# Optimization experiments

Hardware: AMD Instinct MI355X
Metric: run time of the kernel (lower is better)

Reference implementation:

```python
import jax, jax.numpy as jnp
import numpy as np

BS, C, H, W = 256, 512, 9, 9
D = 9           # spe_kerner (spectral attention kernel size)
SPA_HEAD = 64
HW = H * W      # 81; with spe_head=1, padsize=9 => share_head = 81 = HW
EPS = 1e-5


def _bn(x, p, axis=1):
    # inference-mode BatchNorm; p is (4, C) = [gamma, beta, running_mean, running_var]
    g, b, m, v = p
    sh = [1] * x.ndim; sh[axis] = -1
    return (x - m.reshape(sh)) * (g.reshape(sh) * jax.lax.rsqrt(v.reshape(sh) + EPS)) + b.reshape(sh)


def _conv2d(x, w, groups=1):
    return jax.lax.conv_general_dilated(
        x, w, (1, 1), 'SAME',
        dimension_numbers=('NCHW', 'OIHW', 'NCHW'),
        feature_group_count=groups)


def setup_inputs() -> dict:
    key = jax.random.key(0)
    ks = list(jax.random.split(key, 16))

    def rn(k, shape, s=0.05):
        return (jax.random.normal(k, shape) * s).astype(jnp.float32)

    def bnp(k, c):
        k1, k2, k3, k4 = jax.random.split(k, 4)
        g = jax.random.uniform(k1, (c,), minval=0.5, maxval=1.5)
        v = jax.random.uniform(k4, (c,), minval=0.5, maxval=1.5)
        return jnp.stack([g, rn(k2, (c,)), rn(k3, (c,)), v]).astype(jnp.float32)

    return {
        'x': jax.random.normal(ks[0], (BS, C, H, W), jnp.float32),
        'alpha': jnp.full((1,), 0.5, jnp.float32),
        # SaMCA params
        'sa_key_w': rn(ks[1], (C, 1, 3, 3)),                    # depthwise 3x3 key conv
        'sa_key_bn': bnp(ks[2], C),
        'sa_att_w1': rn(ks[3], (C, 2 * C // SPA_HEAD, 1, 1)),   # Conv2d(2C, C, 1, groups=64)
        'sa_att_bn': bnp(ks[4], C),
        'sa_att_w2': rn(ks[5], (SPA_HEAD, C // SPA_HEAD, 1, 1)),  # Conv2d(C, 64, 1, groups=64)
        'sa_att_b2': rn(ks[6], (SPA_HEAD,)),
        # SeMCA params
        'se_key_w': rn(ks[7], (HW, 1, D)),                      # depthwise Conv1d over spectral axis
        'se_key_b': rn(ks[8], (HW,)),
        'se_att_w1': rn(ks[9], (HW, 2 * HW)),                   # 1x1 Conv2d(162, 81), bias=False
        'se_att_bn': bnp(ks[10], HW),
        'se_att_w2': rn(ks[11], (D, HW)),                       # 1x1 Conv2d(81, 9)
        'se_att_b2': rn(ks[12], (D,)),
        'se_val_w': rn(ks[13], (C, 1, 3, 3)),                   # depthwise 3x3 value conv
        'se_val_b': rn(ks[14], (C,)),
    }


def reference(x, alpha, sa_key_w, sa_key_bn, sa_att_w1, sa_att_bn, sa_att_w2,
              sa_att_b2, se_key_w, se_key_b, se_att_w1, se_att_bn, se_att_w2,
              se_att_b2, se_val_w, se_val_b):
    bs, c, h, w = x.shape
    hw = h * w
    # ================= SeMCA (spectral attention) =================
    # convd_key: depthwise Conv1d over the spectral (channel) axis per pixel
    k = x.reshape(bs, c, hw).transpose(0, 2, 1)                 # (bs, hw, c)
    k1 = jax.lax.conv_general_dilated(
        k, se_key_w, (1,), [(D // 2, D // 2)],
        dimension_numbers=('NCH', 'OIH', 'NCH'),
        feature_group_count=hw) + se_key_b[None, :, None]
    k1 = k1.transpose(0, 2, 1).reshape(bs, c, h, w)
    # With padsize==img_size, Unfold(kernel=9) is a single full window -> flatten.
    q_flat = x.reshape(bs, 1, c * hw)
    k_flat = k1.reshape(bs, 1, c * hw)
    # torch layout-faithful: stack on dim 2 then reshape (bs, 2*hw, c)
    kq = jnp.stack([q_flat, k_flat], axis=2).reshape(bs, 2 * hw, c)
    a = jax.nn.relu(_bn(jnp.einsum('oi,bic->boc', se_att_w1, kq), se_att_bn))
    a = jnp.einsum('oi,bic->boc', se_att_w2, a) + se_att_b2[None, :, None]  # (bs, D, c)
    # repeat over all 81 positions + trivial block reshape (sidelen=1) -> same
    # D-vector at every pixel; softmax over the spectral kernel axis.
    a = jax.nn.softmax(a, axis=1)
    v = _conv2d(x, se_val_w, groups=c) + se_val_b[None, :, None, None]
    pad_v = jnp.pad(v, ((0, 0), (D // 2, D // 2), (0, 0), (0, 0)))
    # spectral sliding windows: v_win[b, i, k] = v_padded[b, i + k - D//2]
    v_win = jnp.stack([pad_v[:, k0:k0 + c] for k0 in range(D)], axis=2)  # (bs,c,D,h,w)
    out1 = jnp.einsum('bcdhw,bdc->bchw', v_win, a) + k1
    # ================= SaMCA (spatial attention) =================
    k1s = jax.nn.relu(_bn(_conv2d(x, sa_key_w, groups=c), sa_key_bn))
    # NOTE: value_embed in the original is computed then overwritten by x (dead code).
    kq2 = jnp.stack([k1s, x], axis=2).reshape(bs, 2 * c, h, w)  # interleaved channels
    a2 = jax.nn.relu(_bn(_conv2d(kq2, sa_att_w1, groups=SPA_HEAD), sa_att_bn))
    a2 = _conv2d(a2, sa_att_w2, groups=SPA_HEAD) + sa_att_b2[None, :, None, None]
    a2 = jax.nn.softmax(a2.reshape(bs, SPA_HEAD, hw), axis=-1)  # global spatial softmax
    k2 = jnp.broadcast_to(a2[:, :, None, :], (bs, SPA_HEAD, c // SPA_HEAD, hw)).reshape(bs, c, hw)
    out2 = k1s + (k2 * x.reshape(bs, c, hw)).reshape(bs, c, h, w)
    return alpha * out1 + (1.0 - alpha) * out2
```

## Files before the change

### kernel.cpp

```cpp
#include <hip/hip_runtime.h>
#include <hip/hip_fp16.h>

#define BSZ 256
#define CCH 512
#define HW_ 81
#define DD 9
#define CH 41472

#define WS_W1T   0
#define WS_TSE   13122
#define WS_S2    13203
#define WS_T2    13715
#define WS_W1S   14227
#define WS_T1    22419
#define WS_A2    22932
#define WS_ATT   1350036
#define WS_W1F   2529684
#define WS_TOTALP 22931
#define PREP_N   41363

typedef _Float16 half8 __attribute__((ext_vector_type(8)));
typedef float f32x4 __attribute__((ext_vector_type(4)));

__device__ __forceinline__ float h2f(unsigned short u) {
    return __half2float(__ushort_as_half(u));
}
__device__ __forceinline__ unsigned short f2h(float f) {
    return __half_as_ushort(__float2half(f));
}

__global__ void prep_kernel(const float* __restrict__ se_att_w1,
                            const float* __restrict__ se_att_bn,
                            const float* __restrict__ sa_key_bn,
                            const float* __restrict__ sa_att_w1,
                            const float* __restrict__ sa_att_bn,
                            float* __restrict__ ws) {
    int idx = blockIdx.x * blockDim.x + threadIdx.x;
    if (idx < 13122) {
        int r = idx / 81, o = idx % 81;
        float g = se_att_bn[o], v = se_att_bn[243 + o];
        float s = g * rsqrtf(v + 1e-5f);
        ws[WS_W1T + idx] = se_att_w1[o * 162 + r] * s;
    } else if (idx < 13203) {
        int o = idx - 13122;
        float g = se_att_bn[o], b = se_att_bn[81 + o], m = se_att_bn[162 + o], v = se_att_bn[243 + o];
        float s = g * rsqrtf(v + 1e-5f);
        ws[WS_TSE + o] = b - m * s;
    } else if (idx < 13715) {
        int c = idx - 13203;
        float g = sa_key_bn[c], v = sa_key_bn[1536 + c];
        ws[WS_S2 + c] = g * rsqrtf(v + 1e-5f);
    } else if (idx < 14227) {
        int c = idx - 13715;
        float g = sa_key_bn[c], b = sa_key_bn[512 + c], m = sa_key_bn[1024 + c], v = sa_key_bn[1536 + c];
        float s = g * rsqrtf(v + 1e-5f);
        ws[WS_T2 + c] = b - m * s;
    } else if (idx < 22419) {
        int e = idx - 14227;
        int o = e >> 4;
        float g = sa_att_bn[o], v = sa_att_bn[1536 + o];
        float s = g * rsqrtf(v + 1e-5f);
        ws[WS_W1S + e] = sa_att_w1[e] * s;
    } else if (idx < WS_TOTALP) {
        int o = idx - 22419;
        float g = sa_att_bn[o], b = sa_att_bn[512 + o], m = sa_att_bn[1024 + o], v = sa_att_bn[1536 + o];
        float s = g * rsqrtf(v + 1e-5f);
        ws[WS_T1 + o] = b - m * s;
    } else if (idx < PREP_N) {
        int e2 = (idx - WS_TOTALP) * 2;
        unsigned int packed = 0;
        #pragma unroll
        for (int q = 0; q < 2; ++q) {
            int e = e2 + q;
            int row = e / 192, k = e - row * 192;
            unsigned short val = 0;
            if (row < 81 && k < 162) {
                float g = se_att_bn[row], v = se_att_bn[243 + row];
                float s = g * rsqrtf(v + 1e-5f);
                val = f2h(se_att_w1[row * 162 + k] * s);
            }
            packed |= ((unsigned int)val) << (16 * q);
        }
        ((unsigned int*)(ws + WS_W1F))[idx - WS_TOTALP] = packed;
    }
}

__global__ __launch_bounds__(512, 4) void sa_kernel(
    const float* __restrict__ x,
    const float* __restrict__ sa_key_w,
    const float* __restrict__ sa_att_w2,
    const float* __restrict__ sa_att_b2,
    float* __restrict__ ws)
{
    __shared__ __align__(16) unsigned short xbh[128 * HW_];
    __shared__ float kvf[128 * HW_];
    __shared__ unsigned short wkbL[128 * DD];
    __shared__ float s2L[128];
    __shared__ float t2L[128];
    __shared__ float w1sL[128 * 16];
    __shared__ float saw2L[128];
    __shared__ float b2L[16];
    __shared__ float t1L[128];

    const int bid = blockIdx.x;
    const int b = bid >> 2;
    const int qr = bid & 3;
    const int c0 = qr * 128;
    const int t = threadIdx.x;

    {
        const float4* x4 = (const float4*)(x + (size_t)b * CH + (size_t)c0 * 81);
        for (int v = t; v < 128 * 81 / 4; v += 512) {
            float4 q = x4[v];
            ushort4 s4;
            s4.x = f2h(q.x); s4.y = f2h(q.y); s4.z = f2h(q.z); s4.w = f2h(q.w);
            *(ushort4*)(&xbh[4 * v]) = s4;
        }
        for (int v = t; v < 128 * DD; v += 512) wkbL[v] = f2h(sa_key_w[c0 * 9 + v]);
        if (t < 128) {
            s2L[t] = ws[WS_S2 + c0 + t];
            t2L[t] = ws[WS_T2 + c0 + t];
            saw2L[t] = sa_att_w2[c0 + t];
            t1L[t] = ws[WS_T1 + c0 + t];
        }
        for (int v = t; v < 128 * 16; v += 512) w1sL[v] = ws[WS_W1S + c0 * 16 + v];
        if (t < 16) b2L[t] = sa_att_b2[qr * 16 + t];
    }
    __syncthreads();

    #pragma unroll 2
    for (int idx = t; idx < 128 * 81; idx += 512) {
        int c = idx / 81, p = idx - 81 * c;
        int y = p / 9, xx = p - 9 * y;
        float conv = 0.f;
        #pragma unroll
        for (int ky = 0; ky < 3; ++ky) {
            int yy = y + ky - 1;
            if (yy < 0 || yy > 8) continue;
            #pragma unroll
            for (int kx = 0; kx < 3; ++kx) {
                int xc = xx + kx - 1;
                if (xc < 0 || xc > 8) continue;
                conv = fmaf(h2f(xbh[c * 81 + yy * 9 + xc]),
                            h2f(wkbL[c * 9 + ky * 3 + kx]), conv);
            }
        }
        kvf[idx] = fmaxf(conv * s2L[c] + t2L[c], 0.f);
    }
    __syncthreads();

    {
        const int g = t >> 5, sub = t & 31;
        const int cb = g * 8;
        float z[8][3];
        #pragma unroll
        for (int o = 0; o < 8; ++o)
            #pragma unroll
            for (int k = 0; k < 3; ++k)
                z[o][k] = t1L[cb + o];

        #pragma unroll 1
        for (int j = 0; j < 8; ++j) {
            float wk[8], wx[8];
            #pragma unroll
            for (int o = 0; o < 8; ++o) {
                wk[o] = w1sL[(cb + o) * 16 + 2 * j];
                wx[o] = w1sL[(cb + o) * 16 + 2 * j + 1];
            }
            const int rowb = (cb + j) * 81;
            #pragma unroll
            for (int k = 0; k < 3; ++k) {
                int p = sub + 32 * k;
                if (p > 80) p = 80;
                float kv = kvf[rowb + p];
                float xv = h2f(xbh[rowb + p]);
                #pragma unroll
                for (int o = 0; o < 8; ++o) {
                    z[o][k] = fmaf(wk[o], kv, z[o][k]);
                    z[o][k] = fmaf(wx[o], xv, z[o][k]);
                }
            }
        }

        float a2v[3];
        const float b2g = b2L[g];
        #pragma unroll
        for (int k = 0; k < 3; ++k) {
            float s = b2g;
            #pragma unroll
            for (int o = 0; o < 8; ++o)
                s = fmaf(saw2L[cb + o], fmaxf(z[o][k], 0.f), s);
            int p = sub + 32 * k;
            a2v[k] = (p < 81) ? s : -1e30f;
        }

        float m = a2v[0];
        #pragma unroll
        for (int k = 1; k < 3; ++k) m = fmaxf(m, a2v[k]);
        #pragma unroll
        for (int off = 1; off < 32; off <<= 1) m = fmaxf(m, __shfl_xor(m, off, 64));
        float ls = 0.f;
        float ev[3];
        #pragma unroll
        for (int k = 0; k < 3; ++k) { ev[k] = __expf(a2v[k] - m); ls += ev[k]; }
        #pragma unroll
        for (int off = 1; off < 32; off <<= 1) ls += __shfl_xor(ls, off, 64);
        float inv = 1.f / ls;

        float* a2out = ws + WS_A2 + (size_t)b * 5184 + (size_t)(qr * 16 + g) * 81;
        #pragma unroll
        for (int k = 0; k < 3; ++k) {
            int p = sub + 32 * k;
            if (p < 81) a2out[p] = ev[k] * inv;
        }
    }
}

__global__ __launch_bounds__(512) void se_kernel(
    const float* __restrict__ x,
    const float* __restrict__ se_key_w,
    const float* __restrict__ se_key_b,
    const float* __restrict__ se_att_w2,
    const float* __restrict__ se_att_b2,
    float* __restrict__ ws)
{
    __shared__ __align__(16) unsigned short xbh[CH];
    __shared__ __align__(16) unsigned short kqs[128 * 200];
    __shared__ float wseL[DD * HW_];
    __shared__ float bseL[HW_];
    __shared__ float w2L[DD * 96];
    __shared__ float tseL[96];

    const int b = blockIdx.x;
    const int t = threadIdx.x;
    const float* xb = x + (size_t)b * CH;

    for (int v = t; v < DD * HW_; v += 512) {
        int tau = v / 81, p = v - 81 * tau;
        wseL[tau * 81 + p] = se_key_w[p * 9 + tau];
    }
    if (t < HW_) bseL[t] = se_key_b[t];
    for (int v = t; v < DD * 96; v += 512) {
        int d = v / 96, row = v - 96 * d;
        w2L[v] = (row < 81) ? se_att_w2[d * 81 + row] : 0.f;
    }
    if (t < 96) tseL[t] = (t < 81) ? ws[WS_TSE + t] : 0.f;
    for (int v = t; v < 128 * 38; v += 512) {
        int k = v >> 7, jl = v & 127;
        kqs[jl * 200 + 162 + k] = 0;
    }
    {
        const float4* x4 = (const float4*)xb;
        #pragma unroll 4
        for (int v = t; v < CH / 4; v += 512) {
            float4 q = x4[v];
            ushort4 s4;
            s4.x = f2h(q.x); s4.y = f2h(q.y); s4.z = f2h(q.z); s4.w = f2h(q.w);
            *(ushort4*)(&xbh[4 * v]) = s4;
        }
    }
    __syncthreads();

    const int wv = t >> 6;
    const int lane = t & 63;
    const int quad = lane >> 4;
    const int l15 = lane & 15;
    const unsigned short* w1f = (const unsigned short*)(ws + WS_W1F);
    float* attout = ws + WS_ATT + (size_t)b * 4608;

    #pragma unroll 1
    for (int q = 0; q < 4; ++q) {
        const int c0 = q * 128;
        if (q) __syncthreads();

        {
            int k = t >> 7;
            const int jl = t & 127;
            #pragma unroll 2
            for (; k < 81; k += 4)
                kqs[jl * 200 + k] = xbh[k * 512 + c0 + jl];
        }
        {
            int kk = t >> 7;
            const int jl = t & 127;
            int e = kk * 512 + c0 + jl;
            int p = e % 81;
            #pragma unroll 2
            for (; kk < 81; kk += 4) {
                float s = bseL[p];
                if (e >= 324 && e < CH - 324) {
                    #pragma unroll
                    for (int tau = 0; tau < 9; ++tau)
                        s = fmaf(h2f(xbh[e - 324 + 81 * tau]), wseL[tau * 81 + p], s);
                } else {
                    #pragma unroll
                    for (int tau = 0; tau < 9; ++tau) {
                        int flat = e + (tau - 4) * 81;
                        if (flat >= 0 && flat < CH)
                            s = fmaf(h2f(xbh[flat]), wseL[tau * 81 + p], s);
                    }
                }
                kqs[jl * 200 + 81 + kk] = f2h(s);
                e += 2048;
                p += 23; if (p >= 81) p -= 81;
            }
        }
        __syncthreads();

        f32x4 acc[6];
        #pragma unroll
        for (int m = 0; m < 6; ++m) acc[m] = (f32x4){0.f, 0.f, 0.f, 0.f};

        #pragma unroll 1
        for (int pass = 0; pass < 6; ++pass) {
            half8 bfr = *(const half8*)&kqs[(wv * 16 + l15) * 200 + pass * 32 + quad * 8];
            #pragma unroll
            for (int m = 0; m < 6; ++m) {
                half8 afr = *(const half8*)&w1f[(m * 16 + l15) * 192 + pass * 32 + quad * 8];
                acc[m] = __builtin_amdgcn_mfma_f32_16x16x32_f16(afr, bfr, acc[m], 0, 0, 0);
            }
        }

        float pd[9];
        #pragma unroll
        for (int d = 0; d < 9; ++d) pd[d] = 0.f;
        #pragma unroll
        for (int m = 0; m < 6; ++m) {
            #pragma unroll
            for (int reg = 0; reg < 4; ++reg) {
                int row = m * 16 + quad * 4 + reg;
                float z = fmaxf(acc[m][reg] + tseL[row], 0.f);
                #pragma unroll
                for (int d = 0; d < 9; ++d)
                    pd[d] = fmaf(w2L[d * 96 + row], z, pd[d]);
            }
        }
        #pragma unroll
        for (int d = 0; d < 9; ++d) {
            pd[d] += __shfl_xor(pd[d], 16, 64);
            pd[d] += __shfl_xor(pd[d], 32, 64);
        }
        if (quad == 0) {
            int j = c0 + wv * 16 + l15;
            float ad[9];
            #pragma unroll
            for (int d = 0; d < 9; ++d) ad[d] = pd[d] + se_att_b2[d];
            float mm = ad[0];
            #pragma unroll
            for (int d = 1; d < 9; ++d) mm = fmaxf(mm, ad[d]);
            float ls = 0.f;
            #pragma unroll
            for (int d = 0; d < 9; ++d) { ad[d] = __expf(ad[d] - mm); ls += ad[d]; }
            float inv = 1.f / ls;
            #pragma unroll
            for (int d = 0; d < 9; ++d) attout[d * 512 + j] = ad[d] * inv;
        }
    }
}

#define CS 108
#define RS 12

__device__ __forceinline__ void ldrow_h(const unsigned short* base, float* r) {
    ushort4 a = *(const ushort4*)(base);
    ushort4 bq = *(const ushort4*)(base + 4);
    unsigned short c = base[8];
    r[0] = h2f(a.x); r[1] = h2f(a.y); r[2] = h2f(a.z); r[3] = h2f(a.w);
    r[4] = h2f(bq.x); r[5] = h2f(bq.y); r[6] = h2f(bq.z); r[7] = h2f(bq.w);
    r[8] = h2f(c);
}
__device__ __forceinline__ void ldrow_f(const float* base, float* r) {
    float4 a = *(const float4*)(base);
    float4 bq = *(const float4*)(base + 4);
    r[0] = a.x; r[1] = a.y; r[2] = a.z; r[3] = a.w;
    r[4] = bq.x; r[5] = bq.y; r[6] = bq.z; r[7] = bq.w;
    r[8] = base[8];
}
__device__ __forceinline__ void zrow(float* r) {
    #pragma unroll
    for (int xx = 0; xx < 9; ++xx) r[xx] = 0.f;
}

__global__ __launch_bounds__(256) void combine_kernel(
    const float* __restrict__ x,
    const float* __restrict__ alpha,
    const float* __restrict__ sa_key_w,
    const float* __restrict__ se_key_w,
    const float* __restrict__ se_key_b,
    const float* __restrict__ se_val_w,
    const float* __restrict__ se_val_b,
    const float* __restrict__ ws,
    float* __restrict__ out)
{
    __shared__ __align__(16) unsigned short xsh[72 * CS];
    __shared__ __align__(16) unsigned short vsh[72 * CS];
    __shared__ __align__(16) float wsePad[9 * CS];
    __shared__ __align__(16) float bsePad[CS];
    __shared__ __align__(16) float a2Pad[8 * CS];
    __shared__ float wvL[72 * 9];
    __shared__ float bvL[72];
    __shared__ float wkL[64 * 9];
    __shared__ float s2L[64];
    __shared__ float t2L[64];
    __shared__ float attL[9 * 64];

    const int bid = blockIdx.x;
    const int b = bid >> 3;
    const int tile = bid & 7;
    const int c0 = tile * 64;
    const int t = threadIdx.x;
    const int f0 = (c0 - 4) * 81;

    {
        const float* xg = x + (size_t)b * CH;
        for (int v4 = t; v4 < 1458; v4 += 256) {
            int lf = v4 * 4;
            int gf = f0 + lf;
            float4 q = (gf >= 0 && gf < CH) ? *(const float4*)(xg + gf)
                                            : (float4){0.f, 0.f, 0.f, 0.f};
            #pragma unroll
            for (int j = 0; j < 4; ++j) {
                int lfj = lf + j;
                int i = lfj / 81, p = lfj - 81 * i;
                int yy = p / 9, xx = p - 9 * yy;
                xsh[i * CS + yy * RS + xx] = f2h(((const float*)&q)[j]);
            }
        }
    }
    for (int idx = t; idx < 648; idx += 256) {
        int cc = c0 - 4 + idx / 9;
        wvL[idx] = (cc >= 0 && cc < 512) ? se_val_w[cc * 9 + idx % 9] : 0.f;
    }
    if (t < 72) {
        int cc = c0 - 4 + t;
        bvL[t] = (cc >= 0 && cc < 512) ? se_val_b[cc] : 0.f;
    }
    for (int idx = t; idx < 576; idx += 256) wkL[idx] = sa_key_w[c0 * 9 + idx];
    if (t < 64) { s2L[t] = ws[WS_S2 + c0 + t]; t2L[t] = ws[WS_T2 + c0 + t]; }
    for (int idx = t; idx < 972; idx += 256) {
        int tau = idx / CS, r = idx - CS * tau;
        int yy = r / RS, xx = r - RS * yy;
        if (xx < 9) wsePad[idx] = se_key_w[(yy * 9 + xx) * 9 + tau];
    }
    if (t < CS) {
        int yy = t / RS, xx = t - RS * yy;
        if (xx < 9) bsePad[t] = se_key_b[yy * 9 + xx];
    }
    for (int idx = t; idx < 864; idx += 256) {
        int g = idx / CS, r = idx - CS * g;
        int yy = r / RS, xx = r - RS * yy;
        if (xx < 9)
            a2Pad[idx] = ws[WS_A2 + (size_t)b * 5184 + (size_t)(tile * 8 + g) * 81 + yy * 9 + xx];
    }
    for (int idx = t; idx < 576; idx += 256)
        attL[idx] = ws[WS_ATT + (size_t)b * 4608 + (idx >> 6) * 512 + c0 + (idx & 63)];
    __syncthreads();

    #pragma unroll 1
    for (int u = t; u < 648; u += 256) {
        int i = u / 9, yy = u - 9 * i;
        const int cb = i * CS;
        float q0[9], q1[9], q2[9];
        if (yy > 0) ldrow_h(&xsh[cb + (yy - 1) * RS], q0);
        else zrow(q0);
        ldrow_h(&xsh[cb + yy * RS], q1);
        if (yy < 8) ldrow_h(&xsh[cb + (yy + 1) * RS], q2);
        else zrow(q2);
        float wv[9];
        #pragma unroll
        for (int j = 0; j < 9; ++j) wv[j] = wvL[i * 9 + j];
        const float bv = bvL[i];
        float o[9];
        #pragma unroll
        for (int xx = 0; xx < 9; ++xx) {
            float s = bv;
            #pragma unroll
            for (int kx = 0; kx < 3; ++kx) {
                int xc = xx + kx - 1;
                if (xc >= 0 && xc <= 8) {
                    s = fmaf(q0[xc], wv[kx], s);
                    s = fmaf(q1[xc], wv[3 + kx], s);
                    s = fmaf(q2[xc], wv[6 + kx], s);
                }
            }
            o[xx] = s;
        }
        const int vb = cb + yy * RS;
        ushort4 wA, wB;
        wA.x = f2h(o[0]); wA.y = f2h(o[1]); wA.z = f2h(o[2]); wA.w = f2h(o[3]);
        wB.x = f2h(o[4]); wB.y = f2h(o[5]); wB.z = f2h(o[6]); wB.w = f2h(o[7]);
        *(ushort4*)(&vsh[vb]) = wA;
        *(ushort4*)(&vsh[vb + 4]) = wB;
        vsh[vb + 8] = f2h(o[8]);
    }
    __syncthreads();

    const float av = alpha[0];
    #pragma unroll 1
    for (int u = t; u < 576; u += 256) {
        int cl = u / 9, yy = u - 9 * cl;
        const int rb = yy * RS;
        float acc[9];
        ldrow_f(&bsePad[rb], acc);
        float r1[9];
        #pragma unroll
        for (int tau = 0; tau < 9; ++tau) {
            float xr[9], wr[9];
            ldrow_h(&xsh[(cl + tau) * CS + rb], xr);
            ldrow_f(&wsePad[tau * CS + rb], wr);
            #pragma unroll
            for (int xx = 0; xx < 9; ++xx) acc[xx] = fmaf(xr[xx], wr[xx], acc[xx]);
            if (tau == 4) {
                #pragma unroll
                for (int xx = 0; xx < 9; ++xx) r1[xx] = xr[xx];
            }
        }
        #pragma unroll
        for (int d = 0; d < 9; ++d) {
            float vr[9];
            ldrow_h(&vsh[(cl + d) * CS + rb], vr);
            const float ad = attL[d * 64 + cl];
            #pragma unroll
            for (int xx = 0; xx < 9; ++xx) acc[xx] = fmaf(vr[xx], ad, acc[xx]);
        }
        float r0[9], r2[9];
        if (yy > 0) ldrow_h(&xsh[(cl + 4) * CS + rb - RS], r0);
        else zrow(r0);
        if (yy < 8) ldrow_h(&xsh[(cl + 4) * CS + rb + RS], r2);
        else zrow(r2);
        float wkr[9];
        #pragma unroll
        for (int j = 0; j < 9; ++j) wkr[j] = wkL[cl * 9 + j];
        const float s2 = s2L[cl], t2v = t2L[cl];
        float a2r[9];
        ldrow_f(&a2Pad[(cl >> 3) * CS + rb], a2r);
        float* orow = out + (size_t)b * CH + (size_t)(c0 + cl) * 81 + yy * 9;
        #pragma unroll
        for (int xx = 0; xx < 9; ++xx) {
            float sk = 0.f;
            #pragma unroll
            for (int kx = 0; kx < 3; ++kx) {
                int xc = xx + kx - 1;
                if (xc >= 0 && xc <= 8) {
                    sk = fmaf(r0[xc], wkr[kx], sk);
                    sk = fmaf(r1[xc], wkr[3 + kx], sk);
                    sk = fmaf(r2[xc], wkr[6 + kx], sk);
                }
            }
            float k1s = fmaxf(sk * s2 + t2v, 0.f);
            float out2 = k1s + a2r[xx] * r1[xx];
            orow[xx] = av * acc[xx] + (1.f - av) * out2;
        }
    }
}

extern "C" void kernel_launch(void* const* d_in, const int* in_sizes, int n_in,
                              void* d_out, int out_size, void* d_ws, size_t ws_size,
                              hipStream_t stream) {
    const float* x          = (const float*)d_in[0];
    const float* alpha      = (const float*)d_in[1];
    const float* sa_key_w   = (const float*)d_in[2];
    const float* sa_key_bn  = (const float*)d_in[3];
    const float* sa_att_w1  = (const float*)d_in[4];
    const float* sa_att_bn  = (const float*)d_in[5];
    const float* sa_att_w2  = (const float*)d_in[6];
    const float* sa_att_b2  = (const float*)d_in[7];
    const float* se_key_w   = (const float*)d_in[8];
    const float* se_key_b   = (const float*)d_in[9];
    const float* se_att_w1  = (const float*)d_in[10];
    const float* se_att_bn  = (const float*)d_in[11];
    const float* se_att_w2  = (const float*)d_in[12];
    const float* se_att_b2  = (const float*)d_in[13];
    const float* se_val_w   = (const float*)d_in[14];
    const float* se_val_b   = (const float*)d_in[15];
    float* ws = (float*)d_ws;
    float* outp = (float*)d_out;

    prep_kernel<<<(PREP_N + 255) / 256, 256, 0, stream>>>(
        se_att_w1, se_att_bn, sa_key_bn, sa_att_w1, sa_att_bn, ws);
    sa_kernel<<<BSZ * 4, 512, 0, stream>>>(
        x, sa_key_w, sa_att_w2, sa_att_b2, ws);
    se_kernel<<<BSZ, 512, 0, stream>>>(
        x, se_key_w, se_key_b, se_att_w2, se_att_b2, ws);
    combine_kernel<<<BSZ * 8, 256, 0, stream>>>(
        x, alpha, sa_key_w, se_key_w, se_key_b, se_val_w, se_val_b, ws, outp);
}
```

Before: 291.8 us.

## Split spectral key conv into own kernel and quarter se_kernel per batch

Moves the depthwise spectral key convolution out of se_kernel into a new k1_kernel that writes fp16 results to workspace, computed with 4-wide vectorised LDS reads over a padded tile. se_kernel then launches one block per (batch, 128-channel quarter) instead of one per batch, dropping the full-batch fp16 x staging and the serial 4-quarter loop. This gives four times as many blocks with less LDS each, at the cost of an extra launch and an fp16 round-trip of the key tensor through global memory.

Result: slower. 306.8 us (+5.1%).

```diff
diff --git a/kernel.cpp b/kernel.cpp
--- a/kernel.cpp
+++ b/kernel.cpp
@@ -16,6 +16,7 @@
 #define WS_A2    22932
 #define WS_ATT   1350036
 #define WS_W1F   2529684
+#define WS_K16   2538900
 #define WS_TOTALP 22931
 #define PREP_N   41363
 
@@ -85,6 +86,68 @@
     }
 }
 
+__global__ __launch_bounds__(256) void k1_kernel(
+    const float* __restrict__ x,
+    const float* __restrict__ se_key_w,
+    const float* __restrict__ se_key_b,
+    float* __restrict__ ws)
+{
+    __shared__ __align__(16) unsigned short xpad[136 * 84];
+    __shared__ __align__(16) float wseP[9 * 84];
+    __shared__ __align__(16) float bseP[84];
+
+    const int bid = blockIdx.x;
+    const int b = bid >> 2;
+    const int ct = bid & 3;
+    const int c0 = ct * 128;
+    const int t = threadIdx.x;
+    const float* xb = x + (size_t)b * CH;
+
+    for (int idx = t; idx < 136 * 81; idx += 256) {
+        int r = idx / 81, p = idx - 81 * r;
+        int cc = c0 - 4 + r;
+        float v = (cc >= 0 && cc < 512) ? xb[cc * 81 + p] : 0.f;
+        xpad[r * 84 + p] = f2h(v);
+    }
+    for (int idx = t; idx < 136 * 3; idx += 256) {
+        int r = idx / 3, j = idx - 3 * r;
+        xpad[r * 84 + 81 + j] = 0;
+    }
+    for (int idx = t; idx < 9 * 84; idx += 256) {
+        int tau = idx / 84, p = idx - 84 * tau;
+        wseP[idx] = (p < 81) ? se_key_w[p * 9 + tau] : 0.f;
+    }
+    if (t < 84) bseP[t] = (t < 81) ? se_key_b[t] : 0.f;
+    __syncthreads();
+
+    unsigned short* k16 = (unsigned short*)(ws + WS_K16) + (size_t)b * CH;
+    #pragma unroll 1
+    for (int u = t; u < 128 * 20; u += 256) {
+        int ch = u / 20, g = u - 20 * (u / 20);
+        int p = g * 4;
+        float4 bb = *(const float4*)&bseP[p];
+        float a0 = bb.x, a1 = bb.y, a2 = bb.z, a3 = bb.w;
+        #pragma unroll
+        for (int tau = 0; tau < 9; ++tau) {
+            ushort4 xr = *(const ushort4*)&xpad[(ch + tau) * 84 + p];
+            float4 wr = *(const float4*)&wseP[tau * 84 + p];
+            a0 = fmaf(h2f(xr.x), wr.x, a0);
+            a1 = fmaf(h2f(xr.y), wr.y, a1);
+            a2 = fmaf(h2f(xr.z), wr.z, a2);
+            a3 = fmaf(h2f(xr.w), wr.w, a3);
+        }
+        unsigned short* o = &k16[(size_t)(c0 + ch) * 81 + p];
+        o[0] = f2h(a0); o[1] = f2h(a1); o[2] = f2h(a2); o[3] = f2h(a3);
+    }
+    for (int ch = t; ch < 128; ch += 256) {
+        float a = bseP[80];
+        #pragma unroll
+        for (int tau = 0; tau < 9; ++tau)
+            a = fmaf(h2f(xpad[(ch + tau) * 84 + 80]), wseP[tau * 84 + 80], a);
+        k16[(size_t)(c0 + ch) * 81 + 80] = f2h(a);
+    }
+}
+
 __global__ __launch_bounds__(512, 4) void sa_kernel(
     const float* __restrict__ x,
     const float* __restrict__ sa_key_w,
@@ -218,28 +281,20 @@
 
 __global__ __launch_bounds__(512) void se_kernel(
     const float* __restrict__ x,
-    const float* __restrict__ se_key_w,
-    const float* __restrict__ se_key_b,
     const float* __restrict__ se_att_w2,
     const float* __restrict__ se_att_b2,
     float* __restrict__ ws)
 {
-    __shared__ __align__(16) unsigned short xbh[CH];
     __shared__ __align__(16) unsigned short kqs[128 * 200];
-    __shared__ float wseL[DD * HW_];
-    __shared__ float bseL[HW_];
     __shared__ float w2L[DD * 96];
     __shared__ float tseL[96];
 
-    const int b = blockIdx.x;
+    const int pb = blockIdx.x;
+    const int b = pb >> 2;
+    const int q = pb & 3;
+    const int c0 = q * 128;
     const int t = threadIdx.x;
-    const float* xb = x + (size_t)b * CH;
-
-    for (int v = t; v < DD * HW_; v += 512) {
-        int tau = v / 81, p = v - 81 * tau;
-        wseL[tau * 81 + p] = se_key_w[p * 9 + tau];
-    }
-    if (t < HW_) bseL[t] = se_key_b[t];
+
     for (int v = t; v < DD * 96; v += 512) {
         int d = v / 96, row = v - 96 * d;
         w2L[v] = (row < 81) ? se_att_w2[d * 81 + row] : 0.f;
@@ -250,14 +305,21 @@
         kqs[jl * 200 + 162 + k] = 0;
     }
     {
-        const float4* x4 = (const float4*)xb;
-        #pragma unroll 4
-        for (int v = t; v < CH / 4; v += 512) {
-            float4 q = x4[v];
-            ushort4 s4;
-            s4.x = f2h(q.x); s4.y = f2h(q.y); s4.z = f2h(q.z); s4.w = f2h(q.w);
-            *(ushort4*)(&xbh[4 * v]) = s4;
-        }
+        const float* xb = x + (size_t)b * CH + c0;
+        const int jl = t & 127;
+        int k = t >> 7;
+        #pragma unroll 3
+        for (; k < 81; k += 4)
+            kqs[jl * 200 + k] = f2h(xb[k * 512 + jl]);
+    }
+    {
+        const unsigned short* k16 =
+            (const unsigned short*)(ws + WS_K16) + (size_t)b * CH + c0;
+        const int jl = t & 127;
+        int kk = t >> 7;
+        #pragma unroll 3
+        for (; kk < 81; kk += 4)
+            kqs[jl * 200 + 81 + kk] = k16[kk * 512 + jl];
     }
     __syncthreads();
 
@@ -268,93 +330,53 @@
     const unsigned short* w1f = (const unsigned short*)(ws + WS_W1F);
     float* attout = ws + WS_ATT + (size_t)b * 4608;
 
+    f32x4 acc[6];
+    #pragma unroll
+    for (int m = 0; m < 6; ++m) acc[m] = (f32x4){0.f, 0.f, 0.f, 0.f};
+
     #pragma unroll 1
-    for (int q = 0; q < 4; ++q) {
-        const int c0 = q * 128;
-        if (q) __syncthreads();
-
-        {
-            int k = t >> 7;
-            const int jl = t & 127;
-            #pragma unroll 2
-            for (; k < 81; k += 4)
-                kqs[jl * 200 + k] = xbh[k * 512 + c0 + jl];
-        }
-        {
-            int kk = t >> 7;
-            const int jl = t & 127;
-            int e = kk * 512 + c0 + jl;
-            int p = e % 81;
-            #pragma unroll 2
-            for (; kk < 81; kk += 4) {
-                float s = bseL[p];
-                if (e >= 324 && e < CH - 324) {
-                    #pragma unroll
-                    for (int tau = 0; tau < 9; ++tau)
-                        s = fmaf(h2f(xbh[e - 324 + 81 * tau]), wseL[tau * 81 + p], s);
-                } else {
-                    #pragma unroll
-                    for (int tau = 0; tau < 9; ++tau) {
-                        int flat = e + (tau - 4) * 81;
-                        if (flat >= 0 && flat < CH)
-                            s = fmaf(h2f(xbh[flat]), wseL[tau * 81 + p], s);
-                    }
-                }
-                kqs[jl * 200 + 81 + kk] = f2h(s);
-                e += 2048;
-                p += 23; if (p >= 81) p -= 81;
-            }
-        }
-        __syncthreads();
-
-        f32x4 acc[6];
-        #pragma unroll
-        for (int m = 0; m < 6; ++m) acc[m] = (f32x4){0.f, 0.f, 0.f, 0.f};
-
-        #pragma unroll 1
-        for (int pass = 0; pass < 6; ++pass) {
-            half8 bfr = *(const half8*)&kqs[(wv * 16 + l15) * 200 + pass * 32 + quad * 8];
-            #pragma unroll
-            for (int m = 0; m < 6; ++m) {
-                half8 afr = *(const half8*)&w1f[(m * 16 + l15) * 192 + pass * 32 + quad * 8];
-                acc[m] = __builtin_amdgcn_mfma_f32_16x16x32_f16(afr, bfr, acc[m], 0, 0, 0);
-            }
-        }
-
-        float pd[9];
-        #pragma unroll
-        for (int d = 0; d < 9; ++d) pd[d] = 0.f;
+    for (int pass = 0; pass < 6; ++pass) {
+        half8 bfr = *(const half8*)&kqs[(wv * 16 + l15) * 200 + pass * 32 + quad * 8];
         #pragma unroll
         for (int m = 0; m < 6; ++m) {
-            #pragma unroll
-            for (int reg = 0; reg < 4; ++reg) {
-                int row = m * 16 + quad * 4 + reg;
-                float z = fmaxf(acc[m][reg] + tseL[row], 0.f);
-                #pragma unroll
-                for (int d = 0; d < 9; ++d)
-                    pd[d] = fmaf(w2L[d * 96 + row], z, pd[d]);
-            }
-        }
-        #pragma unroll
-        for (int d = 0; d < 9; ++d) {
-            pd[d] += __shfl_xor(pd[d], 16, 64);
-            pd[d] += __shfl_xor(pd[d], 32, 64);
-        }
-        if (quad == 0) {
-            int j = c0 + wv * 16 + l15;
-            float ad[9];
-            #pragma unroll
-            for (int d = 0; d < 9; ++d) ad[d] = pd[d] + se_att_b2[d];
-            float mm = ad[0];
-            #pragma unroll
-            for (int d = 1; d < 9; ++d) mm = fmaxf(mm, ad[d]);
-            float ls = 0.f;
-            #pragma unroll
-            for (int d = 0; d < 9; ++d) { ad[d] = __expf(ad[d] - mm); ls += ad[d]; }
-            float inv = 1.f / ls;
-            #pragma unroll
-            for (int d = 0; d < 9; ++d) attout[d * 512 + j] = ad[d] * inv;
-        }
+            half8 afr = *(const half8*)&w1f[(m * 16 + l15) * 192 + pass * 32 + quad * 8];
+            acc[m] = __builtin_amdgcn_mfma_f32_16x16x32_f16(afr, bfr, acc[m], 0, 0, 0);
+        }
+    }
+
+    float pd[9];
+    #pragma unroll
+    for (int d = 0; d < 9; ++d) pd[d] = 0.f;
+    #pragma unroll
+    for (int m = 0; m < 6; ++m) {
+        #pragma unroll
+        for (int reg = 0; reg < 4; ++reg) {
+            int row = m * 16 + quad * 4 + reg;
+            float z = fmaxf(acc[m][reg] + tseL[row], 0.f);
+            #pragma unroll
+            for (int d = 0; d < 9; ++d)
+                pd[d] = fmaf(w2L[d * 96 + row], z, pd[d]);
+        }
+    }
+    #pragma unroll
+    for (int d = 0; d < 9; ++d) {
+        pd[d] += __shfl_xor(pd[d], 16, 64);
+        pd[d] += __shfl_xor(pd[d], 32, 64);
+    }
+    if (quad == 0) {
+        int j = c0 + wv * 16 + l15;
+        float ad[9];
+        #pragma unroll
+        for (int d = 0; d < 9; ++d) ad[d] = pd[d] + se_att_b2[d];
+        float mm = ad[0];
+        #pragma unroll
+        for (int d = 1; d < 9; ++d) mm = fmaxf(mm, ad[d]);
+        float ls = 0.f;
+        #pragma unroll
+        for (int d = 0; d < 9; ++d) { ad[d] = __expf(ad[d] - mm); ls += ad[d]; }
+        float inv = 1.f / ls;
+        #pragma unroll
+        for (int d = 0; d < 9; ++d) attout[d * 512 + j] = ad[d] * inv;
     }
 }
 
@@ -578,10 +600,12 @@
 
     prep_kernel<<<(PREP_N + 255) / 256, 256, 0, stream>>>(
         se_att_w1, se_att_bn, sa_key_bn, sa_att_w1, sa_att_bn, ws);
+    k1_kernel<<<BSZ * 4, 256, 0, stream>>>(
+        x, se_key_w, se_key_b, ws);
     sa_kernel<<<BSZ * 4, 512, 0, stream>>>(
         x, sa_key_w, sa_att_w2, sa_att_b2, ws);
-    se_kernel<<<BSZ, 512, 0, stream>>>(
-        x, se_key_w, se_key_b, se_att_w2, se_att_b2, ws);
+    se_kernel<<<BSZ * 4, 512, 0, stream>>>(
+        x, se_att_w2, se_att_b2, ws);
     combine_kernel<<<BSZ * 8, 256, 0, stream>>>(
         x, alpha, sa_key_w, se_key_w, se_key_b, se_val_w, se_val_b, ws, outp);
 }
```
